# Kernel optimization log

Hardware: AMD Instinct MI355X
Metric: run time of the kernel (lower is better)

Reference implementation:

```python
import jax, jax.numpy as jnp
import numpy as np

FRAME_LEN = 512
FRAME_HOP = 256
EPSILON = float(np.finfo(np.float32).eps)


def _dft_kernels(frame_len=FRAME_LEN):
    # Matches torch: K = view_as_real(fft.rfft(eye(N), dim=1))[:frame_len], windowed by hann.
    # rfft of delta at t gives exp(-2pi i f t / N): real = cos, imag = -sin.
    N = frame_len  # already a power of two
    n = jnp.arange(frame_len, dtype=jnp.float32)
    window = 0.5 * (1.0 - jnp.cos(2.0 * jnp.pi * n / frame_len))  # periodic hann
    f = jnp.arange(N // 2 + 1, dtype=jnp.float32)  # 257 bins
    ang = 2.0 * jnp.pi * f[:, None] * n[None, :] / N  # [F, L]
    Kr = jnp.cos(ang) * window
    Ki = -jnp.sin(ang) * window  # torch rfft imaginary part
    return Kr, Ki


def _frame(x, frame_len=FRAME_LEN, hop=FRAME_HOP):
    B, Ns = x.shape
    T = (Ns - frame_len) // hop + 1
    idx = jnp.arange(T)[:, None] * hop + jnp.arange(frame_len)[None, :]  # [T, L]
    return x[:, idx]  # [B, T, L]


def reference(x):
    Kr, Ki = _dft_kernels()
    xf = _frame(x)  # [B, T, L]
    r = jnp.einsum('btl,fl->bft', xf, Kr)       # real part of conv1d output
    i = -jnp.einsum('btl,fl->bft', xf, Ki)      # i = -imag (as in torch code)
    mag = jnp.sqrt(r * r + i * i)               # B x F x T
    f = jnp.clip(mag, EPSILON, None)
    mean = jnp.mean(f, axis=-1, keepdims=True)
    std = jnp.std(f, axis=-1, keepdims=True, ddof=1)  # torch std is unbiased
    feat = (f - mean) / (std + EPSILON)
    return mag, feat


def setup_inputs() -> dict:
    key = jax.random.key(0)
    x = jax.random.normal(key, (64, 160000), dtype=jnp.float32)
    return {"x": x}
```

## Files before the change

### kernel.cpp

```cpp
#include <hip/hip_runtime.h>
#include <math.h>

#define FRAME_LEN 512
#define HOP       256
#define NFREQ     257
#define NFREQ_PAD 288
#define NBATCH    64
#define NSAMP     160000
#define TFRAMES   624
#define EPS       1.1920928955078125e-07f

#define MT 128
#define FT 32
#define BK 64
#define NK (FRAME_LEN / BK)
#define NXCD 8
#define XBLKS 5000

typedef __attribute__((ext_vector_type(8))) short short8;
typedef __attribute__((ext_vector_type(4))) float f32x4;

static __device__ __forceinline__ unsigned int f2bf(float f) {
    unsigned int u = __float_as_uint(f);
    return (u + 0x7fffu + ((u >> 16) & 1u)) >> 16;
}
static __device__ __forceinline__ uint4 pack8(float4 a, float4 b) {
    uint4 r;
    r.x = f2bf(a.x) | (f2bf(a.y) << 16);
    r.y = f2bf(a.z) | (f2bf(a.w) << 16);
    r.z = f2bf(b.x) | (f2bf(b.y) << 16);
    r.w = f2bf(b.z) | (f2bf(b.w) << 16);
    return r;
}
static __device__ __forceinline__ void gload_lds16(const void* g, void* l) {
    __builtin_amdgcn_global_load_lds(
        (const __attribute__((address_space(1))) void*)g,
        (__attribute__((address_space(3))) void*)l, 16, 0, 0);
}

__global__ __launch_bounds__(256) void prep(const float* __restrict__ x,
                                            unsigned short* __restrict__ xbf,
                                            unsigned short* __restrict__ Wc,
                                            unsigned short* __restrict__ Ws) {
    if (blockIdx.x < XBLKS) {
        int i = blockIdx.x * 256 + threadIdx.x;
        const float4* src = (const float4*)x + (size_t)i * 2;
        float4 a = src[0], b = src[1];
        *(uint4*)(xbf + (size_t)i * 8) = pack8(a, b);
    } else {
        int f = blockIdx.x - XBLKS;
        for (int n = threadIdx.x; n < FRAME_LEN; n += 256) {
            unsigned short c = 0, s = 0;
            if (f < NFREQ) {
                float w = 0.5f * (1.0f - cosf(2.0f * (float)M_PI * (float)n / (float)FRAME_LEN));
                int r = (f * n) & (FRAME_LEN - 1);
                float ang = (float)r * (2.0f * (float)M_PI / (float)FRAME_LEN);
                float sv, cv;
                sincosf(ang, &sv, &cv);
                c = (unsigned short)f2bf(cv * w);
                s = (unsigned short)f2bf(sv * w);
            }
            Wc[f * FRAME_LEN + n] = c;
            Ws[f * FRAME_LEN + n] = s;
        }
    }
}

__global__ __launch_bounds__(256) void stft_mfma(
    const unsigned short* __restrict__ xbf, const unsigned short* __restrict__ Wc,
    const unsigned short* __restrict__ Ws, float* __restrict__ mag)
{
    __shared__ unsigned short As[2][MT][BK];
    __shared__ unsigned short Bs[2][2][FT][BK];

    const int tid = threadIdx.x;
    const int logical = (blockIdx.x % NXCD) * (2808 / NXCD) + blockIdx.x / NXCD;
    const int tileM = logical / 9;
    const int tileF = logical % 9;
    const int wid = tid >> 6;
    const int lane = tid & 63;
    const int lrow = lane & 15;
    const int lhi = lane >> 4;

    const unsigned short* pA[4];
    #pragma unroll
    for (int j = 0; j < 4; j++) {
        int idx = wid * 4 + j;
        int row = idx * 8 + (lane >> 3);
        int m = tileM * MT + row;
        int b = m / TFRAMES;
        int t = m - b * TFRAMES;
        int chunk = (lane & 7) ^ (row & 7);
        pA[j] = xbf + (size_t)b * NSAMP + t * HOP + chunk * 8;
    }
    const unsigned short* pB[2];
    #pragma unroll
    for (int j = 0; j < 2; j++) {
        int i = wid * 2 + j;
        int row = (i & 3) * 8 + (lane >> 3);
        int f = tileF * FT + row;
        int chunk = (lane & 7) ^ (row & 7);
        const unsigned short* tbl = (i & 4) ? Ws : Wc;
        pB[j] = tbl + f * FRAME_LEN + chunk * 8;
    }

    f32x4 accr[2][2] = {};
    f32x4 acci[2][2] = {};

    #pragma unroll
    for (int j = 0; j < 4; j++)
        gload_lds16(pA[j], (unsigned short*)As[0] + (wid * 4 + j) * 512);
    #pragma unroll
    for (int j = 0; j < 2; j++)
        gload_lds16(pB[j], (unsigned short*)Bs[0] + (wid * 2 + j) * 512);
    __syncthreads();

    for (int it = 0; it < NK; it++) {
        const int cur = it & 1;
        if (it < NK - 1) {
            const int k0 = (it + 1) * BK;
            #pragma unroll
            for (int j = 0; j < 4; j++)
                gload_lds16(pA[j] + k0, (unsigned short*)As[cur ^ 1] + (wid * 4 + j) * 512);
            #pragma unroll
            for (int j = 0; j < 2; j++)
                gload_lds16(pB[j] + k0, (unsigned short*)Bs[cur ^ 1] + (wid * 2 + j) * 512);
        }
        #pragma unroll
        for (int ks = 0; ks < 2; ks++) {
            short8 a[2], bc[2], bsn[2];
            const int c = (ks * 4 + lhi) ^ (lrow & 7);
            #pragma unroll
            for (int mf = 0; mf < 2; mf++)
                a[mf] = *(const short8*)&As[cur][wid * 32 + mf * 16 + lrow][c * 8];
            #pragma unroll
            for (int nf = 0; nf < 2; nf++) {
                bc[nf]  = *(const short8*)&Bs[cur][0][nf * 16 + lrow][c * 8];
                bsn[nf] = *(const short8*)&Bs[cur][1][nf * 16 + lrow][c * 8];
            }
            #pragma unroll
            for (int mf = 0; mf < 2; mf++) {
                #pragma unroll
                for (int nf = 0; nf < 2; nf++) {
                    accr[mf][nf] = __builtin_amdgcn_mfma_f32_16x16x32_bf16(
                        a[mf], bc[nf], accr[mf][nf], 0, 0, 0);
                    acci[mf][nf] = __builtin_amdgcn_mfma_f32_16x16x32_bf16(
                        a[mf], bsn[nf], acci[mf][nf], 0, 0, 0);
                }
            }
        }
        __syncthreads();
    }

    #pragma unroll
    for (int mf = 0; mf < 2; mf++) {
        int m0 = tileM * MT + wid * 32 + mf * 16 + lhi * 4;
        int b = m0 / TFRAMES;
        int t = m0 - b * TFRAMES;
        #pragma unroll
        for (int nf = 0; nf < 2; nf++) {
            int f = tileF * FT + nf * 16 + lrow;
            if (f < NFREQ) {
                float4 o;
                o.x = sqrtf(accr[mf][nf][0] * accr[mf][nf][0] + acci[mf][nf][0] * acci[mf][nf][0]);
                o.y = sqrtf(accr[mf][nf][1] * accr[mf][nf][1] + acci[mf][nf][1] * acci[mf][nf][1]);
                o.z = sqrtf(accr[mf][nf][2] * accr[mf][nf][2] + acci[mf][nf][2] * acci[mf][nf][2]);
                o.w = sqrtf(accr[mf][nf][3] * accr[mf][nf][3] + acci[mf][nf][3] * acci[mf][nf][3]);
                *(float4*)(mag + ((size_t)b * NFREQ + f) * TFRAMES + t) = o;
            }
        }
    }
}

__global__ __launch_bounds__(256) void normalize(const float* __restrict__ mag,
                                                 float* __restrict__ feat)
{
    const int row = blockIdx.x * 4 + (threadIdx.x >> 6);
    const int lane = threadIdx.x & 63;
    const float* mp = mag + (size_t)row * TFRAMES;

    float4 v[3];
    float sum = 0.f;
    #pragma unroll
    for (int i = 0; i < 3; i++) {
        int c4 = lane + i * 64;
        if (c4 < TFRAMES / 4) {
            float4 t = *(const float4*)(mp + c4 * 4);
            t.x = fmaxf(t.x, EPS); t.y = fmaxf(t.y, EPS);
            t.z = fmaxf(t.z, EPS); t.w = fmaxf(t.w, EPS);
            v[i] = t;
            sum += (t.x + t.y) + (t.z + t.w);
        } else {
            v[i] = make_float4(0.f, 0.f, 0.f, 0.f);
        }
    }
    #pragma unroll
    for (int off = 1; off < 64; off <<= 1) sum += __shfl_xor(sum, off, 64);
    const float mean = sum * (1.0f / (float)TFRAMES);

    float ssd = 0.f;
    #pragma unroll
    for (int i = 0; i < 3; i++) {
        int c4 = lane + i * 64;
        if (c4 < TFRAMES / 4) {
            float dx = v[i].x - mean, dy = v[i].y - mean;
            float dz = v[i].z - mean, dw = v[i].w - mean;
            ssd += (dx * dx + dy * dy) + (dz * dz + dw * dw);
        }
    }
    #pragma unroll
    for (int off = 1; off < 64; off <<= 1) ssd += __shfl_xor(ssd, off, 64);
    const float stdv = sqrtf(ssd * (1.0f / (float)(TFRAMES - 1)));
    const float inv = 1.0f / (stdv + EPS);

    float* fp = feat + (size_t)row * TFRAMES;
    #pragma unroll
    for (int i = 0; i < 3; i++) {
        int c4 = lane + i * 64;
        if (c4 < TFRAMES / 4) {
            float4 o;
            o.x = (v[i].x - mean) * inv; o.y = (v[i].y - mean) * inv;
            o.z = (v[i].z - mean) * inv; o.w = (v[i].w - mean) * inv;
            *(float4*)(fp + c4 * 4) = o;
        }
    }
}

extern "C" void kernel_launch(void* const* d_in, const int* in_sizes, int n_in,
                              void* d_out, int out_size, void* d_ws, size_t ws_size,
                              hipStream_t stream) {
    const float* x = (const float*)d_in[0];
    unsigned short* Wc  = (unsigned short*)d_ws;
    unsigned short* Ws  = Wc + NFREQ_PAD * FRAME_LEN;
    unsigned short* xbf = Ws + NFREQ_PAD * FRAME_LEN;
    float* mag  = (float*)d_out;
    float* feat = mag + (size_t)NBATCH * NFREQ * TFRAMES;

    prep<<<XBLKS + NFREQ_PAD, 256, 0, stream>>>(x, xbf, Wc, Ws);

    stft_mfma<<<312 * 9, 256, 0, stream>>>(xbf, Wc, Ws, mag);

    normalize<<<NBATCH * NFREQ / 4, 256, 0, stream>>>(mag, feat);
}
```

Before: 61.49 us.

## Use radix-4 decimation to compute only 65 base bins and derive the rest

The input is split into four polyphase streams (sample index mod 4) during the bf16 conversion. The DFT matrix is reduced to 65 frequencies of length-128 decimated kernels. The MFMA kernel accumulates four partial cos/sin sums, one per phase, and combines them with radix-4 butterflies in the epilogue to produce bins f, 128-f, 128+f and 256-f. This cuts the GEMM FLOPs and the tile count by about three times, at the cost of more accumulator registers and scattered output writes.

```diff
diff --git a/kernel.cpp b/kernel.cpp
--- a/kernel.cpp
+++ b/kernel.cpp
@@ -4,18 +4,22 @@
 #define FRAME_LEN 512
 #define HOP       256
 #define NFREQ     257
-#define NFREQ_PAD 288
 #define NBATCH    64
 #define NSAMP     160000
+#define NSQ       40000
 #define TFRAMES   624
 #define EPS       1.1920928955078125e-07f
 
 #define MT 128
 #define FT 32
 #define BK 64
-#define NK (FRAME_LEN / BK)
-#define NXCD 8
-#define XBLKS 5000
+#define RS 2560000
+#define TS 12288
+#define TBLKS 96
+#define XBLKS 2500
+
+#define ASZ (MT * BK)
+#define BSZ (2 * FT * BK)
 
 typedef __attribute__((ext_vector_type(8))) short short8;
 typedef __attribute__((ext_vector_type(4))) float f32x4;
@@ -23,14 +27,6 @@
 static __device__ __forceinline__ unsigned int f2bf(float f) {
     unsigned int u = __float_as_uint(f);
     return (u + 0x7fffu + ((u >> 16) & 1u)) >> 16;
-}
-static __device__ __forceinline__ uint4 pack8(float4 a, float4 b) {
-    uint4 r;
-    r.x = f2bf(a.x) | (f2bf(a.y) << 16);
-    r.y = f2bf(a.z) | (f2bf(a.w) << 16);
-    r.z = f2bf(b.x) | (f2bf(b.y) << 16);
-    r.w = f2bf(b.z) | (f2bf(b.w) << 16);
-    return r;
 }
 static __device__ __forceinline__ void gload_lds16(const void* g, void* l) {
     __builtin_amdgcn_global_load_lds(
@@ -39,48 +35,68 @@
 }
 
 __global__ __launch_bounds__(256) void prep(const float* __restrict__ x,
-                                            unsigned short* __restrict__ xbf,
-                                            unsigned short* __restrict__ Wc,
-                                            unsigned short* __restrict__ Ws) {
-    if (blockIdx.x < XBLKS) {
-        int i = blockIdx.x * 256 + threadIdx.x;
-        const float4* src = (const float4*)x + (size_t)i * 2;
-        float4 a = src[0], b = src[1];
-        *(uint4*)(xbf + (size_t)i * 8) = pack8(a, b);
-    } else {
-        int f = blockIdx.x - XBLKS;
-        for (int n = threadIdx.x; n < FRAME_LEN; n += 256) {
-            unsigned short c = 0, s = 0;
-            if (f < NFREQ) {
+                                            unsigned short* __restrict__ xq,
+                                            unsigned short* __restrict__ Wt) {
+    if (blockIdx.x < TBLKS) {
+        const int f = blockIdx.x;
+        #pragma unroll
+        for (int h = 0; h < 2; h++) {
+            const int n = threadIdx.x + h * 256;
+            unsigned short cb = 0, sb = 0;
+            if (f <= 64) {
                 float w = 0.5f * (1.0f - cosf(2.0f * (float)M_PI * (float)n / (float)FRAME_LEN));
-                int r = (f * n) & (FRAME_LEN - 1);
-                float ang = (float)r * (2.0f * (float)M_PI / (float)FRAME_LEN);
+                float ang = (float)((f * n) & (FRAME_LEN - 1)) * (2.0f * (float)M_PI / (float)FRAME_LEN);
                 float sv, cv;
                 sincosf(ang, &sv, &cv);
-                c = (unsigned short)f2bf(cv * w);
-                s = (unsigned short)f2bf(sv * w);
-            }
-            Wc[f * FRAME_LEN + n] = c;
-            Ws[f * FRAME_LEN + n] = s;
-        }
+                cb = (unsigned short)f2bf(cv * w);
+                sb = (unsigned short)f2bf(sv * w);
+            }
+            const int r = n & 3, q = n >> 2;
+            Wt[(r * 2 + 0) * TS + f * 128 + q] = cb;
+            Wt[(r * 2 + 1) * TS + f * 128 + q] = sb;
+        }
+    } else {
+        const int i = (blockIdx.x - TBLKS) * 256 + threadIdx.x;
+        const int g = i * 16;
+        const int b = g / NSAMP;
+        const int s = g - b * NSAMP;
+        const float4* src = (const float4*)(x + (size_t)b * NSAMP + s);
+        const float4 v0 = src[0], v1 = src[1], v2 = src[2], v3 = src[3];
+        const size_t o = (size_t)b * NSQ + (s >> 2);
+        uint2 p;
+        p.x = f2bf(v0.x) | (f2bf(v1.x) << 16);
+        p.y = f2bf(v2.x) | (f2bf(v3.x) << 16);
+        *(uint2*)(xq + 0 * (size_t)RS + o) = p;
+        p.x = f2bf(v0.y) | (f2bf(v1.y) << 16);
+        p.y = f2bf(v2.y) | (f2bf(v3.y) << 16);
+        *(uint2*)(xq + 1 * (size_t)RS + o) = p;
+        p.x = f2bf(v0.z) | (f2bf(v1.z) << 16);
+        p.y = f2bf(v2.z) | (f2bf(v3.z) << 16);
+        *(uint2*)(xq + 2 * (size_t)RS + o) = p;
+        p.x = f2bf(v0.w) | (f2bf(v1.w) << 16);
+        p.y = f2bf(v2.w) | (f2bf(v3.w) << 16);
+        *(uint2*)(xq + 3 * (size_t)RS + o) = p;
     }
 }
 
 __global__ __launch_bounds__(256) void stft_mfma(
-    const unsigned short* __restrict__ xbf, const unsigned short* __restrict__ Wc,
-    const unsigned short* __restrict__ Ws, float* __restrict__ mag)
+    const unsigned short* __restrict__ xq, const unsigned short* __restrict__ Wt,
+    float* __restrict__ mag)
 {
     __shared__ unsigned short As[2][MT][BK];
     __shared__ unsigned short Bs[2][2][FT][BK];
 
     const int tid = threadIdx.x;
-    const int logical = (blockIdx.x % NXCD) * (2808 / NXCD) + blockIdx.x / NXCD;
-    const int tileM = logical / 9;
-    const int tileF = logical % 9;
+    const int logical = ((int)blockIdx.x & 7) * 117 + ((int)blockIdx.x >> 3);
+    const int tileM = logical / 3;
+    const int tileF = logical % 3;
     const int wid = tid >> 6;
     const int lane = tid & 63;
     const int lrow = lane & 15;
     const int lhi = lane >> 4;
+
+    unsigned short* AsB = &As[0][0][0];
+    unsigned short* BsB = &Bs[0][0][0][0];
 
     const unsigned short* pA[4];
     #pragma unroll
@@ -91,40 +107,44 @@
         int b = m / TFRAMES;
         int t = m - b * TFRAMES;
         int chunk = (lane & 7) ^ (row & 7);
-        pA[j] = xbf + (size_t)b * NSAMP + t * HOP + chunk * 8;
+        pA[j] = xq + (size_t)b * NSQ + t * (HOP / 4) + chunk * 8;
     }
     const unsigned short* pB[2];
     #pragma unroll
     for (int j = 0; j < 2; j++) {
         int i = wid * 2 + j;
         int row = (i & 3) * 8 + (lane >> 3);
-        int f = tileF * FT + row;
+        int fg = tileF * FT + row;
         int chunk = (lane & 7) ^ (row & 7);
-        const unsigned short* tbl = (i & 4) ? Ws : Wc;
-        pB[j] = tbl + f * FRAME_LEN + chunk * 8;
-    }
-
-    f32x4 accr[2][2] = {};
-    f32x4 acci[2][2] = {};
+        pB[j] = Wt + ((i & 4) ? TS : 0) + fg * 128 + chunk * 8;
+    }
+
+    f32x4 aC[4][2][2] = {};
+    f32x4 aS[4][2][2] = {};
 
     #pragma unroll
     for (int j = 0; j < 4; j++)
-        gload_lds16(pA[j], (unsigned short*)As[0] + (wid * 4 + j) * 512);
+        gload_lds16(pA[j], AsB + (wid * 4 + j) * 512);
     #pragma unroll
     for (int j = 0; j < 2; j++)
-        gload_lds16(pB[j], (unsigned short*)Bs[0] + (wid * 2 + j) * 512);
+        gload_lds16(pB[j], BsB + (wid * 2 + j) * 512);
     __syncthreads();
 
-    for (int it = 0; it < NK; it++) {
-        const int cur = it & 1;
-        if (it < NK - 1) {
-            const int k0 = (it + 1) * BK;
+    int buf = 0;
+    #pragma unroll
+    for (int it = 0; it < 8; it++) {
+        const int R = it >> 1;
+        if (it < 7) {
+            const int Rn = (it + 1) >> 1;
+            const int kn = ((it + 1) & 1) * BK;
+            const size_t aoff = (size_t)Rn * RS + kn;
+            const size_t boff = (size_t)Rn * (2 * TS) + kn;
             #pragma unroll
             for (int j = 0; j < 4; j++)
-                gload_lds16(pA[j] + k0, (unsigned short*)As[cur ^ 1] + (wid * 4 + j) * 512);
+                gload_lds16(pA[j] + aoff, AsB + (buf ^ 1) * ASZ + (wid * 4 + j) * 512);
             #pragma unroll
             for (int j = 0; j < 2; j++)
-                gload_lds16(pB[j] + k0, (unsigned short*)Bs[cur ^ 1] + (wid * 2 + j) * 512);
+                gload_lds16(pB[j] + boff, BsB + (buf ^ 1) * BSZ + (wid * 2 + j) * 512);
         }
         #pragma unroll
         for (int ks = 0; ks < 2; ks++) {
@@ -132,24 +152,28 @@
             const int c = (ks * 4 + lhi) ^ (lrow & 7);
             #pragma unroll
             for (int mf = 0; mf < 2; mf++)
-                a[mf] = *(const short8*)&As[cur][wid * 32 + mf * 16 + lrow][c * 8];
+                a[mf] = *(const short8*)(AsB + buf * ASZ +
+                    (wid * 32 + mf * 16 + lrow) * BK + c * 8);
             #pragma unroll
             for (int nf = 0; nf < 2; nf++) {
-                bc[nf]  = *(const short8*)&Bs[cur][0][nf * 16 + lrow][c * 8];
-                bsn[nf] = *(const short8*)&Bs[cur][1][nf * 16 + lrow][c * 8];
+                bc[nf]  = *(const short8*)(BsB + buf * BSZ +
+                    (nf * 16 + lrow) * BK + c * 8);
+                bsn[nf] = *(const short8*)(BsB + buf * BSZ + FT * BK +
+                    (nf * 16 + lrow) * BK + c * 8);
             }
             #pragma unroll
             for (int mf = 0; mf < 2; mf++) {
                 #pragma unroll
                 for (int nf = 0; nf < 2; nf++) {
-                    accr[mf][nf] = __builtin_amdgcn_mfma_f32_16x16x32_bf16(
-                        a[mf], bc[nf], accr[mf][nf], 0, 0, 0);
-                    acci[mf][nf] = __builtin_amdgcn_mfma_f32_16x16x32_bf16(
-                        a[mf], bsn[nf], acci[mf][nf], 0, 0, 0);
+                    aC[R][mf][nf] = __builtin_amdgcn_mfma_f32_16x16x32_bf16(
+                        a[mf], bc[nf], aC[R][mf][nf], 0, 0, 0);
+                    aS[R][mf][nf] = __builtin_amdgcn_mfma_f32_16x16x32_bf16(
+                        a[mf], bsn[nf], aS[R][mf][nf], 0, 0, 0);
                 }
             }
         }
         __syncthreads();
+        buf ^= 1;
     }
 
     #pragma unroll
@@ -157,17 +181,31 @@
         int m0 = tileM * MT + wid * 32 + mf * 16 + lhi * 4;
         int b = m0 / TFRAMES;
         int t = m0 - b * TFRAMES;
+        float* magb = mag + (size_t)b * NFREQ * TFRAMES + t;
         #pragma unroll
         for (int nf = 0; nf < 2; nf++) {
             int f = tileF * FT + nf * 16 + lrow;
-            if (f < NFREQ) {
-                float4 o;
-                o.x = sqrtf(accr[mf][nf][0] * accr[mf][nf][0] + acci[mf][nf][0] * acci[mf][nf][0]);
-                o.y = sqrtf(accr[mf][nf][1] * accr[mf][nf][1] + acci[mf][nf][1] * acci[mf][nf][1]);
-                o.z = sqrtf(accr[mf][nf][2] * accr[mf][nf][2] + acci[mf][nf][2] * acci[mf][nf][2]);
-                o.w = sqrtf(accr[mf][nf][3] * accr[mf][nf][3] + acci[mf][nf][3] * acci[mf][nf][3]);
-                *(float4*)(mag + ((size_t)b * NFREQ + f) * TFRAMES + t) = o;
-            }
+            float4 o1, o2, o3, o4;
+            #pragma unroll
+            for (int q = 0; q < 4; q++) {
+                const float C0 = aC[0][mf][nf][q], C1 = aC[1][mf][nf][q];
+                const float C2 = aC[2][mf][nf][q], C3 = aC[3][mf][nf][q];
+                const float S0 = aS[0][mf][nf][q], S1 = aS[1][mf][nf][q];
+                const float S2 = aS[2][mf][nf][q], S3 = aS[3][mf][nf][q];
+                float r, i2;
+                r = (C0 + C2) + (C1 + C3); i2 = (S0 + S2) + (S1 + S3);
+                (&o1.x)[q] = sqrtf(r * r + i2 * i2);
+                r = (C0 - C2) + (S1 - S3); i2 = (C1 - C3) - (S0 - S2);
+                (&o2.x)[q] = sqrtf(r * r + i2 * i2);
+                r = (C0 - C2) - (S1 - S3); i2 = (C1 - C3) + (S0 - S2);
+                (&o3.x)[q] = sqrtf(r * r + i2 * i2);
+                r = (C0 + C2) - (C1 + C3); i2 = (S1 + S3) - (S0 + S2);
+                (&o4.x)[q] = sqrtf(r * r + i2 * i2);
+            }
+            if (f <= 64)           *(float4*)(magb + (size_t)f * TFRAMES) = o1;
+            if (f <= 63)           *(float4*)(magb + (size_t)(128 - f) * TFRAMES) = o2;
+            if (f >= 1 && f <= 64) *(float4*)(magb + (size_t)(128 + f) * TFRAMES) = o3;
+            if (f <= 63)           *(float4*)(magb + (size_t)(256 - f) * TFRAMES) = o4;
         }
     }
 }
@@ -230,15 +268,14 @@
                               void* d_out, int out_size, void* d_ws, size_t ws_size,
                               hipStream_t stream) {
     const float* x = (const float*)d_in[0];
-    unsigned short* Wc  = (unsigned short*)d_ws;
-    unsigned short* Ws  = Wc + NFREQ_PAD * FRAME_LEN;
-    unsigned short* xbf = Ws + NFREQ_PAD * FRAME_LEN;
+    unsigned short* Wt = (unsigned short*)d_ws;
+    unsigned short* xq = Wt + 8 * TS;
     float* mag  = (float*)d_out;
     float* feat = mag + (size_t)NBATCH * NFREQ * TFRAMES;
 
-    prep<<<XBLKS + NFREQ_PAD, 256, 0, stream>>>(x, xbf, Wc, Ws);
-
-    stft_mfma<<<312 * 9, 256, 0, stream>>>(xbf, Wc, Ws, mag);
+    prep<<<TBLKS + XBLKS, 256, 0, stream>>>(x, xq, Wt);
+
+    stft_mfma<<<312 * 3, 256, 0, stream>>>(xq, Wt, mag);
 
     normalize<<<NBATCH * NFREQ / 4, 256, 0, stream>>>(mag, feat);
 }
```

After: 51.89 us (median of 2 runs). 15.6% less time.
